# Kernel tuning notes

Measured on AMD Instinct MI355X. Metric: run time of the kernel, lower is better.

The kernel has to match this reference:

```python
import jax, jax.numpy as jnp
import numpy as np

KSIZE = 13
BETA = 0.97
THR = 1.0
SMIN, SMAX = 0.4, 10.0


def gaussian_kernel(sigma):
    # matches torch: coarse grid [-6,6] (13 pts), normalized by sum over fine grid [-60,60] (130 pts)
    r = jnp.linspace(-(KSIZE // 2), KSIZE // 2, KSIZE)
    r_all = jnp.linspace(-(KSIZE // 2) * 10.0, (KSIZE // 2) * 10.0, KSIZE * 10)
    k = jnp.exp(-0.5 * (r / sigma) ** 2)
    norm = jnp.sum(jnp.exp(-0.5 * (r_all / sigma) ** 2))
    return k / norm


def setup_inputs() -> dict:
    key = jax.random.key(0)
    k1, = jax.random.split(key, 1)
    B, C, T = 512, 224, 224
    inp = jax.random.normal(k1, (B, 1, C, T), dtype=jnp.float32)
    w = jnp.float32((SMIN + SMAX) / 2.0)  # 5.2, init value of nn.Parameter
    return {"inp": inp, "w": w}


def reference(inp, w):
    x = inp[:, 0]                      # (B, C, T)
    B, C, T = x.shape
    wc = jnp.clip(w, SMIN, SMAX)
    kern = gaussian_kernel(wc)          # (K,), symmetric
    pad = (KSIZE - 1) // 2

    # gaussian smoothing across the channel axis, same kernel for every t and b
    # x_mean[b,c,t] = sum_k kern[k] * pad_C(x)[b, c+k, t]
    xc = x.transpose(0, 2, 1).reshape(B * T, 1, C)   # (B*T, 1, C)
    xm = jax.lax.conv_general_dilated(
        xc, kern.reshape(1, 1, KSIZE),
        window_strides=(1,), padding=[(pad, pad)],
        dimension_numbers=("NCH", "OIH", "NCH"))
    x_mean = xm.reshape(B, T, C).transpose(0, 2, 1)  # (B, C, T)

    # input current: clip x at the smoothed mean from above
    I = x - jax.nn.relu(x - x_mean)                   # (B, C, T)

    # snn.Leaky (beta=0.97, threshold=1, reset_mechanism='subtract')
    def step(mem, I_t):
        reset = (mem > THR).astype(mem.dtype)         # reset based on previous mem
        mem = BETA * mem + I_t - reset * THR
        spk = (mem > THR).astype(mem.dtype)           # Heaviside(mem - threshold)
        return mem, spk

    mem0 = jnp.zeros((B, C), x.dtype)
    _, spk = jax.lax.scan(step, mem0, I.transpose(2, 0, 1))  # (T, B, C)
    spk = spk.transpose(1, 2, 0)[:, None]                    # (B, 1, C, T)
    return spk
```

## Files before the change

### kernel.cpp

```cpp
#include <hip/hip_runtime.h>

constexpr int Cc  = 224;
constexpr int Tt  = 224;
constexpr int KS  = 13;
constexpr int PAD = 6;
constexpr int TT  = 32;
constexpr int LDW = TT + 1;
constexpr int ROWS = Cc + 2 * PAD;
constexpr int BDIM = 256;

__global__ __launch_bounds__(BDIM)
void cgss_snn_kernel(const float* __restrict__ x,
                     const float* __restrict__ wp,
                     float* __restrict__ out)
{
    __shared__ float kern[KS];
    __shared__ float tile[ROWS * LDW];
    __shared__ float otile[Cc * LDW];

    const int tid = threadIdx.x;
    const int b   = blockIdx.x;
    const long long base = (long long)b * Cc * Tt;

    for (int idx = tid; idx < 2 * PAD * LDW; idx += BDIM) {
        int row = idx / LDW;
        int col = idx - row * LDW;
        int r   = (row < PAD) ? row : (row + Cc);
        tile[r * LDW + col] = 0.0f;
    }

    if (tid == 0) {
        float w  = wp[0];
        float wc = fminf(fmaxf(w, 0.4f), 10.0f);
        float norm = 0.0f;
        const float step = 120.0f / 129.0f;
        for (int j = 0; j < KS * 10; ++j) {
            float r = -60.0f + (float)j * step;
            float z = r / wc;
            norm += expf(-0.5f * z * z);
        }
        for (int i = 0; i < KS; ++i) {
            float r = (float)(i - PAD);
            float z = r / wc;
            kern[i] = expf(-0.5f * z * z) / norm;
        }
    }
    __syncthreads();

    float kr[KS];
#pragma unroll
    for (int i = 0; i < KS; ++i) kr[i] = kern[i];

    const int c = tid;
    float mem = 0.0f;
    float rst = 0.0f;

    for (int t0 = 0; t0 < Tt; t0 += TT) {
#pragma unroll
        for (int r = 0; r < (Cc * TT / 4) / BDIM; ++r) {
            int q  = r * BDIM + tid;
            int cc = q >> 3;
            int tq = (q & 7) << 2;
            const float4 v = *reinterpret_cast<const float4*>(
                x + base + (long long)cc * Tt + t0 + tq);
            int la = (cc + PAD) * LDW + tq;
            tile[la + 0] = v.x; tile[la + 1] = v.y;
            tile[la + 2] = v.z; tile[la + 3] = v.w;
        }
        __syncthreads();

        if (c < Cc) {
#pragma unroll 4
            for (int t = 0; t < TT; ++t) {
                float acc = 0.0f;
#pragma unroll
                for (int i = 0; i < KS; ++i)
                    acc += kr[i] * tile[(c + i) * LDW + t];
                float xv = tile[(c + PAD) * LDW + t];
                float d  = xv - acc;
                float rl = d > 0.0f ? d : 0.0f;
                float I  = xv - rl;
                mem = 0.97f * mem + I - rst;
                float spk = (mem > 1.0f) ? 1.0f : 0.0f;
                rst = spk;
                otile[c * LDW + t] = spk;
            }
        }
        __syncthreads();

        for (int q = tid; q < Cc * TT; q += BDIM) {
            int cc = q >> 5;
            int t  = q & 31;
            out[base + (long long)cc * Tt + t0 + t] = otile[cc * LDW + t];
        }
        __syncthreads();
    }
}

extern "C" void kernel_launch(void* const* d_in, const int* in_sizes, int n_in,
                              void* d_out, int out_size, void* d_ws, size_t ws_size,
                              hipStream_t stream)
{
    const float* x  = (const float*)d_in[0];
    const float* w  = (const float*)d_in[1];
    float* out      = (float*)d_out;
    const int B = in_sizes[0] / (Cc * Tt);
    cgss_snn_kernel<<<B, BDIM, 0, stream>>>(x, w, out);
}
```

Baseline: 68.62 us.

## Rewrite SNN kernel with per-wave async LDS double buffering and register blocking

```diff
diff --git a/kernel.cpp b/kernel.cpp
--- a/kernel.cpp
+++ b/kernel.cpp
@@ -1,99 +1,150 @@
 #include <hip/hip_runtime.h>
 
-constexpr int Cc  = 224;
-constexpr int Tt  = 224;
-constexpr int KS  = 13;
-constexpr int PAD = 6;
-constexpr int TT  = 32;
-constexpr int LDW = TT + 1;
-constexpr int ROWS = Cc + 2 * PAD;
-constexpr int BDIM = 256;
+constexpr int Cc = 224;
+constexpr int Tt = 224;
+constexpr int TT = 32;
+constexpr int NTILE = Tt / TT;
+constexpr int SROWS = 128;
+constexpr int SLABWORDS = SROWS * TT;
+constexpr int BDIM = 128;
+
+#define GLDS16(src, dst) __builtin_amdgcn_global_load_lds( \
+    (const __attribute__((address_space(1))) unsigned int*)(src), \
+    (__attribute__((address_space(3))) unsigned int*)(dst), 16, 0, 0)
 
 __global__ __launch_bounds__(BDIM)
 void cgss_snn_kernel(const float* __restrict__ x,
                      const float* __restrict__ wp,
                      float* __restrict__ out)
 {
-    __shared__ float kern[KS];
-    __shared__ float tile[ROWS * LDW];
-    __shared__ float otile[Cc * LDW];
+    __shared__ float lds[2 * 2 * SLABWORDS];
 
     const int tid = threadIdx.x;
+    const int w   = tid >> 6;
+    const int l   = tid & 63;
     const int b   = blockIdx.x;
-    const long long base = (long long)b * Cc * Tt;
 
-    for (int idx = tid; idx < 2 * PAD * LDW; idx += BDIM) {
-        int row = idx / LDW;
-        int col = idx - row * LDW;
-        int r   = (row < PAD) ? row : (row + Cc);
-        tile[r * LDW + col] = 0.0f;
+    float* slab = &lds[w * 2 * SLABWORDS];
+    const long long bofs = (long long)b * Cc * Tt;
+    const float* xb = x + bofs;
+    float*       ob = out + bofs;
+
+    const int cbase = 112 * w - 8;
+
+    {
+        const int zj = (w == 0) ? 0 : 15;
+        float4 z = make_float4(0.f, 0.f, 0.f, 0.f);
+        *reinterpret_cast<float4*>(&slab[0 * SLABWORDS + zj * 256 + l * 4]) = z;
+        *reinterpret_cast<float4*>(&slab[1 * SLABWORDS + zj * 256 + l * 4]) = z;
     }
 
-    if (tid == 0) {
-        float w  = wp[0];
-        float wc = fminf(fmaxf(w, 0.4f), 10.0f);
+    const int jbeg = (w == 0) ? 1 : 0;
+    const int jend = (w == 0) ? 16 : 15;
+    const int srow = l >> 3;
+    const int sc   = l & 7;
+
+    auto stage = [&](int buf, int t0) {
+        for (int j = jbeg; j < jend; ++j) {
+            int r  = 8 * j + srow;
+            int tq = sc ^ ((r >> 1) & 7);
+            const float* src = xb + (cbase + r) * Tt + t0 + tq * 4;
+            float* dst = &slab[buf * SLABWORDS + j * 256];
+            GLDS16(src, dst);
+        }
+    };
+
+    stage(0, 0);
+
+    float kr[13];
+    {
+        float wv = wp[0];
+        float wc = fminf(fmaxf(wv, 0.4f), 10.0f);
         float norm = 0.0f;
         const float step = 120.0f / 129.0f;
-        for (int j = 0; j < KS * 10; ++j) {
+        for (int j = 0; j < 130; ++j) {
             float r = -60.0f + (float)j * step;
             float z = r / wc;
             norm += expf(-0.5f * z * z);
         }
-        for (int i = 0; i < KS; ++i) {
-            float r = (float)(i - PAD);
+        for (int i = 0; i < 13; ++i) {
+            float r = (float)(i - 6);
             float z = r / wc;
-            kern[i] = expf(-0.5f * z * z) / norm;
+            kr[i] = expf(-0.5f * z * z) / norm;
         }
     }
-    __syncthreads();
 
-    float kr[KS];
+    float mem0 = 0.f, mem1 = 0.f, rst0 = 0.f, rst1 = 0.f;
+    const int c0 = 112 * w + 2 * l;
+    int buf = 0;
+
+    asm volatile("s_waitcnt vmcnt(0)" ::: "memory");
+    __builtin_amdgcn_sched_barrier(0);
+
+    for (int tile = 0; tile < NTILE; ++tile) {
+        const int t0 = tile * TT;
+        if (tile < NTILE - 1) stage(buf ^ 1, t0 + TT);
+
+        if (l < 56) {
+            const float* sb = &slab[buf * SLABWORDS];
+            const int rb = 2 * l + 2;
+#pragma unroll 2
+            for (int tq = 0; tq < 8; ++tq) {
+                float4 val[14];
 #pragma unroll
-    for (int i = 0; i < KS; ++i) kr[i] = kern[i];
-
-    const int c = tid;
-    float mem = 0.0f;
-    float rst = 0.0f;
-
-    for (int t0 = 0; t0 < Tt; t0 += TT) {
+                for (int k = 0; k < 14; ++k) {
+                    int r = rb + k;
+                    int q = tq ^ ((r >> 1) & 7);
+                    val[k] = *reinterpret_cast<const float4*>(&sb[r * 32 + q * 4]);
+                }
+                float4 a0 = make_float4(0,0,0,0), a1 = make_float4(0,0,0,0);
 #pragma unroll
-        for (int r = 0; r < (Cc * TT / 4) / BDIM; ++r) {
-            int q  = r * BDIM + tid;
-            int cc = q >> 3;
-            int tq = (q & 7) << 2;
-            const float4 v = *reinterpret_cast<const float4*>(
-                x + base + (long long)cc * Tt + t0 + tq);
-            int la = (cc + PAD) * LDW + tq;
-            tile[la + 0] = v.x; tile[la + 1] = v.y;
-            tile[la + 2] = v.z; tile[la + 3] = v.w;
-        }
-        __syncthreads();
-
-        if (c < Cc) {
-#pragma unroll 4
-            for (int t = 0; t < TT; ++t) {
-                float acc = 0.0f;
+                for (int i = 0; i < 13; ++i) {
+                    float kk = kr[i];
+                    a0.x += kk * val[i].x;    a0.y += kk * val[i].y;
+                    a0.z += kk * val[i].z;    a0.w += kk * val[i].w;
+                    a1.x += kk * val[i+1].x;  a1.y += kk * val[i+1].y;
+                    a1.z += kk * val[i+1].z;  a1.w += kk * val[i+1].w;
+                }
+                float4 s0, s1;
+                {
+                    const float* xv = (const float*)&val[6];
+                    const float* av = (const float*)&a0;
+                    float*       sv = (float*)&s0;
 #pragma unroll
-                for (int i = 0; i < KS; ++i)
-                    acc += kr[i] * tile[(c + i) * LDW + t];
-                float xv = tile[(c + PAD) * LDW + t];
-                float d  = xv - acc;
-                float rl = d > 0.0f ? d : 0.0f;
-                float I  = xv - rl;
-                mem = 0.97f * mem + I - rst;
-                float spk = (mem > 1.0f) ? 1.0f : 0.0f;
-                rst = spk;
-                otile[c * LDW + t] = spk;
+                    for (int s = 0; s < 4; ++s) {
+                        float d  = xv[s] - av[s];
+                        float rl = d > 0.0f ? d : 0.0f;
+                        float I  = xv[s] - rl;
+                        mem0 = 0.97f * mem0 + I - rst0;
+                        float spk = (mem0 > 1.0f) ? 1.0f : 0.0f;
+                        rst0 = spk;
+                        sv[s] = spk;
+                    }
+                }
+                {
+                    const float* xv = (const float*)&val[7];
+                    const float* av = (const float*)&a1;
+                    float*       sv = (float*)&s1;
+#pragma unroll
+                    for (int s = 0; s < 4; ++s) {
+                        float d  = xv[s] - av[s];
+                        float rl = d > 0.0f ? d : 0.0f;
+                        float I  = xv[s] - rl;
+                        mem1 = 0.97f * mem1 + I - rst1;
+                        float spk = (mem1 > 1.0f) ? 1.0f : 0.0f;
+                        rst1 = spk;
+                        sv[s] = spk;
+                    }
+                }
+                const int t = t0 + tq * 4;
+                *reinterpret_cast<float4*>(&ob[(long long)c0 * Tt + t])       = s0;
+                *reinterpret_cast<float4*>(&ob[(long long)(c0 + 1) * Tt + t]) = s1;
             }
         }
-        __syncthreads();
 
-        for (int q = tid; q < Cc * TT; q += BDIM) {
-            int cc = q >> 5;
-            int t  = q & 31;
-            out[base + (long long)cc * Tt + t0 + t] = otile[cc * LDW + t];
-        }
-        __syncthreads();
+        asm volatile("s_waitcnt vmcnt(0)" ::: "memory");
+        __builtin_amdgcn_sched_barrier(0);
+        buf ^= 1;
     }
 }
 
```

Result: faster. 67.26 us (-2.0%).
